# Performance work log

Hardware: AMD Instinct MI355X
Metric: run time of the kernel (lower is better)

## Reference

```python
import jax, jax.numpy as jnp
import numpy as np

N, E, NFEAT, NHID, NCLASS = 50000, 800000, 8, 128, 112
SMOOTH = 0.5          # smoo init arg
NEG_SLOPE_ATT = 0.2   # LeakyReLU slope inside sparse attention (SpGAT convention)
NEG_SLOPE_OUT = 0.01  # F.leaky_relu default in the outer loop
EPS = 1e-16


def setup_inputs() -> dict:
    key = jax.random.key(0)
    ks = jax.random.split(key, 12)
    g = lambda k, shape, s=0.1: jax.random.normal(k, shape, dtype=jnp.float32) * s
    return {
        "x": jax.random.normal(ks[0], (N, NFEAT), dtype=jnp.float32),
        "edge_index": jax.random.randint(ks[1], (2, E), 0, N, dtype=jnp.int64) if jax.config.jax_enable_x64 else jax.random.randint(ks[1], (2, E), 0, N, dtype=jnp.int32),
        "edge_weight": jax.random.uniform(ks[2], (E,), dtype=jnp.float32),
        # ScattterAttentionLayer 1: nfeat -> nhid (weight W, attention vector a split into src/dst halves)
        "W1": g(ks[3], (NFEAT, NHID)),
        "a1_src": g(ks[4], (NHID,)),
        "a1_dst": g(ks[5], (NHID,)),
        # ScattterAttentionLayer 2: nhid -> nhid
        "W2": g(ks[6], (NHID, NHID)),
        "a2_src": g(ks[7], (NHID,)),
        "a2_dst": g(ks[8], (NHID,)),
        # shared BatchNorm1d(nhid)
        "gamma": jnp.ones((NHID,), jnp.float32),
        "beta": jnp.zeros((NHID,), jnp.float32),
        # GC_withres: nhid -> nclass
        "Wg": g(ks[9], (NHID, NCLASS)),
        "bg": jnp.zeros((NCLASS,), jnp.float32),
    }


def scatter_attention(h_in, W, a_src, a_dst, src, dst):
    """Sparse GAT-style scatter attention (SpGraphAttentionLayer math).
    score_ij = exp(-leakyrelu(a_src.h_i + a_dst.h_j)); softmax-normalized per dst node."""
    h = h_in @ W                                   # [N, F]
    f_src = h @ a_src                              # [N]
    f_dst = h @ a_dst                              # [N]
    e = jnp.exp(-jax.nn.leaky_relu(f_src[src] + f_dst[dst], NEG_SLOPE_ATT))  # [E]
    denom = jax.ops.segment_sum(e, dst, num_segments=N) + EPS                # [N]
    num = jax.ops.segment_sum(e[:, None] * h[src], dst, num_segments=N)      # [N, F]
    return num / denom[:, None]


def batchnorm(x, gamma, beta):
    mu = x.mean(axis=0)
    var = x.var(axis=0)
    return (x - mu) * jax.lax.rsqrt(var + 1e-5) * gamma + beta


def reference(x, edge_index, edge_weight, W1, a1_src, a1_dst, W2, a2_src, a2_dst, gamma, beta, Wg, bg):
    src, dst = edge_index[0], edge_index[1]
    # conv loop (nlayers=3 -> two ScattterAttentionLayer convs), shared bn1, leaky_relu; dropout=identity (eval)
    h = scatter_attention(x, W1, a1_src, a1_dst, src, dst)
    h = jax.nn.leaky_relu(batchnorm(h, gamma, beta), NEG_SLOPE_OUT)
    h = scatter_attention(h, W2, a2_src, a2_dst, src, dst)
    h = jax.nn.leaky_relu(batchnorm(h, gamma, beta), NEG_SLOPE_OUT)
    # GC_withres: spmm((smooth*A + I)/(1+smooth), h @ Wg) + bias
    support = h @ Wg                               # [N, nclass]
    w = (SMOOTH / (1.0 + SMOOTH)) * edge_weight    # [E]
    agg = jax.ops.segment_sum(w[:, None] * support[src], dst, num_segments=N)
    return agg + support / (1.0 + SMOOTH) + bg
```

## Files before the change

### kernel.cpp

```cpp
#include <hip/hip_runtime.h>
#include <hip/hip_bf16.h>

#define N_NODES 50000
#define N_EDGES 800000
#define NFEAT   8
#define NHID    128
#define NCLASS  112
#define SEG_EPS 1e-16f
#define BN_EPS  1e-5f
#define CAP     64
#define MACRO_TILES 782
#define NODE_RANGE 6250
#define FILL_CHUNK 2048
#define FILL_CHUNKS 391
#define FSFD_BLOCKS 196
#define GATH_GRID 12800
#define ATT_GRID 3200
#define ATT_IT 4
#define Y1_BLOCKS 256

typedef __hip_bfloat16 bf16;
typedef __attribute__((ext_vector_type(8))) short short8;
typedef __attribute__((ext_vector_type(4))) float f32x4;
typedef __attribute__((ext_vector_type(4))) unsigned int u32x4;

__device__ __forceinline__ float bfbits2f(unsigned int lo16) {
    union { unsigned int u; float f; } c; c.u = lo16 << 16; return c.f;
}

__device__ __forceinline__ unsigned int pack_bf2(float a, float b) {
    union { unsigned int u; bf16 h[2]; } t;
    t.h[0] = __float2bfloat16(a);
    t.h[1] = __float2bfloat16(b);
    return t.u;
}

__global__ __launch_bounds__(256)
void k_fill_fsfd(const int* __restrict__ src, const int* __restrict__ dst,
                 const float* __restrict__ ewt,
                 int* __restrict__ cnt, unsigned int* __restrict__ bucket,
                 const float* __restrict__ x, const float* __restrict__ W1,
                 const float* __restrict__ a1s, const float* __restrict__ a1d,
                 float* __restrict__ fs, float* __restrict__ fd) {
    if (blockIdx.x < FILL_CHUNKS * 8) {
        const int range = blockIdx.x & 7;
        const int chunk = blockIdx.x >> 3;
        const int lo = range * NODE_RANGE, hi = lo + NODE_RANGE;
        const int e0 = chunk * FILL_CHUNK + threadIdx.x * 8;
        if (e0 >= N_EDGES) return;
        const int4 d0 = *(const int4*)&dst[e0];
        const int4 d1 = *(const int4*)&dst[e0 + 4];
        const int dd[8] = {d0.x, d0.y, d0.z, d0.w, d1.x, d1.y, d1.z, d1.w};
#pragma unroll
        for (int i = 0; i < 8; i++) {
            int d = dd[i];
            if (d < lo || d >= hi) continue;
            int e = e0 + i;
            int slot = atomicAdd(&cnt[d], 1);
            if (slot < CAP) {
                unsigned int iw = (unsigned int)(ewt[e] * 32767.f + 0.5f);
                bucket[d * CAP + slot] = ((unsigned int)src[e] << 15) | iw;
            }
        }
        return;
    }
    __shared__ float sw[16];
    const int t = threadIdx.x, w = t >> 6, lane = t & 63;
#pragma unroll
    for (int dd = 0; dd < 4; dd++) {
        int dot = w + dd * 4;
        int k = dot & 7;
        const float* a = (dot < 8) ? a1s : a1d;
        float v = W1[k * NHID + lane] * a[lane] + W1[k * NHID + 64 + lane] * a[64 + lane];
#pragma unroll
        for (int off = 32; off > 0; off >>= 1) v += __shfl_down(v, off);
        if (lane == 0) sw[dot] = v;
    }
    __syncthreads();
    const int i = (blockIdx.x - FILL_CHUNKS * 8) * 256 + t;
    if (i < N_NODES) {
        const float4 x0 = ((const float4*)x)[i * 2];
        const float4 x1 = ((const float4*)x)[i * 2 + 1];
        fs[i] = x0.x*sw[0] + x0.y*sw[1] + x0.z*sw[2] + x0.w*sw[3]
              + x1.x*sw[4] + x1.y*sw[5] + x1.z*sw[6] + x1.w*sw[7];
        fd[i] = x0.x*sw[8] + x0.y*sw[9] + x0.z*sw[10] + x0.w*sw[11]
              + x1.x*sw[12] + x1.y*sw[13] + x1.z*sw[14] + x1.w*sw[15];
    }
}

__global__ __launch_bounds__(256)
void k_sort_gather_x(const int* __restrict__ cnt, unsigned int* __restrict__ bucket,
                     const float* __restrict__ fs, const float* __restrict__ fd,
                     const float* __restrict__ x, float* __restrict__ xaggn) {
    const int xcd = blockIdx.x & 7;
    const int wb  = blockIdx.x >> 3;
    const int ni  = wb * 4 + (threadIdx.x >> 6);
    if (ni >= NODE_RANGE) return;
    const int d = xcd * NODE_RANGE + ni;
    const int lane = threadIdx.x & 63;
    const int deg = min(cnt[d], CAP);
    unsigned int v = (lane < deg) ? bucket[d * CAP + lane] : 0xFFFFFFFFu;
#pragma unroll
    for (int k = 2; k <= 64; k <<= 1) {
#pragma unroll
        for (int s = k >> 1; s > 0; s >>= 1) {
            unsigned int o = (unsigned int)__shfl_xor((int)v, s);
            bool keepmin = ((lane & s) == 0) == ((lane & k) == 0);
            v = keepmin ? min(v, o) : max(v, o);
        }
    }
    if (lane < deg) bucket[d * CAP + lane] = v;
    const int epair = lane >> 1;
    const int half  = lane & 1;
    const float fdd = fd[d];
    float4 acc = {0.f, 0.f, 0.f, 0.f};
    float den = 0.f;
    for (int base = 0; base < deg; base += 32) {
        int e = base + epair;
        unsigned int u = (unsigned int)__shfl((int)v, e);
        if (e < deg) {
            int s = u >> 15;
            float f = fs[s] + fdd;
            float lr = f > 0.f ? f : 0.2f * f;
            float c = __expf(-lr);
            if (half == 0) den += c;
            const float4 xv = *(const float4*)&x[s * NFEAT + half * 4];
            acc.x += c * xv.x; acc.y += c * xv.y; acc.z += c * xv.z; acc.w += c * xv.w;
        }
    }
#pragma unroll
    for (int off = 2; off < 64; off <<= 1) {
        acc.x += __shfl_xor(acc.x, off);
        acc.y += __shfl_xor(acc.y, off);
        acc.z += __shfl_xor(acc.z, off);
        acc.w += __shfl_xor(acc.w, off);
        den   += __shfl_xor(den, off);
    }
    den += __shfl_xor(den, 1);
    if (lane < 2) {
        float r = 1.f / (den + SEG_EPS);
        float4 o;
        o.x = acc.x * r; o.y = acc.y * r; o.z = acc.z * r; o.w = acc.w * r;
        *(float4*)&xaggn[d * NFEAT + half * 4] = o;
    }
}

__global__ __launch_bounds__(256)
void k_y1_gemm(const float* __restrict__ xaggn, const float* __restrict__ W1,
               bf16* __restrict__ y1, float* __restrict__ Psum, float* __restrict__ Psq) {
    int t = threadIdx.x;
    int r = t >> 7, j = t & 127;
    float w[NFEAT];
#pragma unroll
    for (int k = 0; k < NFEAT; k++) w[k] = W1[k * NHID + j];
    float ls = 0.f, lq = 0.f;
    for (int row = blockIdx.x * 2 + r; row < N_NODES; row += gridDim.x * 2) {
        const float4 x0 = ((const float4*)xaggn)[row * 2];
        const float4 x1 = ((const float4*)xaggn)[row * 2 + 1];
        float v = x0.x*w[0] + x0.y*w[1] + x0.z*w[2] + x0.w*w[3]
                + x1.x*w[4] + x1.y*w[5] + x1.z*w[6] + x1.w*w[7];
        y1[(size_t)row * NHID + j] = __float2bfloat16(v);
        ls += v; lq += v * v;
    }
    __shared__ float sbuf[256];
    sbuf[t] = ls; __syncthreads();
    if (r == 0) Psum[blockIdx.x * 128 + j] = sbuf[j] + sbuf[j + 128];
    __syncthreads();
    sbuf[t] = lq; __syncthreads();
    if (r == 0) Psq[blockIdx.x * 128 + j] = sbuf[j] + sbuf[j + 128];
}

__global__ __launch_bounds__(512)
void k_bn_w2(const float* __restrict__ Psum, const float* __restrict__ Psq,
             const float* __restrict__ gamma, const float* __restrict__ beta,
             float* __restrict__ scale, float* __restrict__ shift,
             const float* __restrict__ W2,
             const float* __restrict__ as_, const float* __restrict__ ad_,
             float* __restrict__ ws_, float* __restrict__ wd_) {
    const int t = threadIdx.x;
    if (blockIdx.x == 0) {
        int j = t & 127;
        int g = t >> 7;
        float s = 0.f, q = 0.f;
#pragma unroll 8
        for (int b = g * 64; b < g * 64 + 64; b++) {
            s += Psum[b * 128 + j];
            q += Psq[b * 128 + j];
        }
        __shared__ float Ls[4][128], Lq[4][128];
        Ls[g][j] = s; Lq[g][j] = q;
        __syncthreads();
        if (g == 0) {
            float st = ((Ls[0][j] + Ls[1][j]) + Ls[2][j]) + Ls[3][j];
            float qt = ((Lq[0][j] + Lq[1][j]) + Lq[2][j]) + Lq[3][j];
            float mu = st * (1.f / N_NODES);
            float var = qt * (1.f / N_NODES) - mu * mu;
            float rs = rsqrtf(var + BN_EPS);
            float ga = gamma[j];
            scale[j] = rs * ga;
            shift[j] = beta[j] - mu * rs * ga;
        }
        return;
    }
    const int k = (blockIdx.x - 1) * 4 + (t >> 7);
    const int n = t & 127;
    float wv = W2[k * NHID + n];
    float vs = wv * as_[n], vd = wv * ad_[n];
#pragma unroll
    for (int off = 32; off > 0; off >>= 1) { vs += __shfl_down(vs, off); vd += __shfl_down(vd, off); }
    __shared__ float ps[8], pd[8];
    const int wid = t >> 6;
    if ((t & 63) == 0) { ps[wid] = vs; pd[wid] = vd; }
    __syncthreads();
    if ((t & 127) == 0) { ws_[k] = ps[wid] + ps[wid + 1]; wd_[k] = pd[wid] + pd[wid + 1]; }
}

__global__ __launch_bounds__(256)
void k_reduce_a(const float* __restrict__ Psum, const float* __restrict__ Psq,
                int nIn, int chunk,
                float* __restrict__ Qsum, float* __restrict__ Qsq) {
    int j = threadIdx.x & 127;
    int h = threadIdx.x >> 7;
    int u = blockIdx.x * 2 + h;
    int b0 = u * chunk, b1 = min(b0 + chunk, nIn);
    float s = 0.f, q = 0.f;
#pragma unroll 8
    for (int b = b0; b < b1; b++) {
        s += Psum[b * 128 + j];
        q += Psq[b * 128 + j];
    }
    Qsum[u * 128 + j] = s;
    Qsq[u * 128 + j] = q;
}

__global__ __launch_bounds__(512)
void k_reduce_b(const float* __restrict__ Qsum, const float* __restrict__ Qsq,
                const float* __restrict__ gamma, const float* __restrict__ beta,
                float* __restrict__ scale, float* __restrict__ shift) {
    int j = threadIdx.x & 127;
    int g = threadIdx.x >> 7;
    float s = 0.f, q = 0.f;
#pragma unroll
    for (int u = g * 8; u < g * 8 + 8; u++) {
        s += Qsum[u * 128 + j];
        q += Qsq[u * 128 + j];
    }
    __shared__ float Ls[4][128], Lq[4][128];
    Ls[g][j] = s; Lq[g][j] = q;
    __syncthreads();
    if (g == 0) {
        float st = ((Ls[0][j] + Ls[1][j]) + Ls[2][j]) + Ls[3][j];
        float qt = ((Lq[0][j] + Lq[1][j]) + Lq[2][j]) + Lq[3][j];
        float mu = st * (1.f / N_NODES);
        float var = qt * (1.f / N_NODES) - mu * mu;
        float rs = rsqrtf(var + BN_EPS);
        float ga = gamma[j];
        scale[j] = rs * ga;
        shift[j] = beta[j] - mu * rs * ga;
    }
}

template<int NCV, int OSTRIDE, bool ATT>
__global__ __launch_bounds__(256)
void k_gemm_mfma(const bf16* __restrict__ Yin,
                 const float* __restrict__ scale, const float* __restrict__ shift,
                 const float* __restrict__ W,
                 bf16* __restrict__ hout,
                 const float* __restrict__ w2s, const float* __restrict__ w2d,
                 float* __restrict__ fs, float* __restrict__ fd) {
    constexpr int NT = NCV / 16;
    constexpr int NC4 = NCV / 4;
    __shared__ bf16 Wt[NCV * 136];
    __shared__ bf16 At[64 * 136];
    const int t = threadIdx.x;
    for (int idx = t; idx < 128 * NC4; idx += 256) {
        int k = idx / NC4, n4 = (idx - k * NC4) * 4;
        const float4 wv = *(const float4*)&W[k * NCV + n4];
        Wt[(n4 + 0) * 136 + k] = __float2bfloat16(wv.x);
        Wt[(n4 + 1) * 136 + k] = __float2bfloat16(wv.y);
        Wt[(n4 + 2) * 136 + k] = __float2bfloat16(wv.z);
        Wt[(n4 + 3) * 136 + k] = __float2bfloat16(wv.w);
    }
    const int chunk = t & 15;
    const int rgrp  = t >> 4;
    float sc[8], sh[8];
    {
        const float4 s0 = *(const float4*)&scale[chunk * 8];
        const float4 s1 = *(const float4*)&scale[chunk * 8 + 4];
        const float4 h0 = *(const float4*)&shift[chunk * 8];
        const float4 h1 = *(const float4*)&shift[chunk * 8 + 4];
        sc[0]=s0.x; sc[1]=s0.y; sc[2]=s0.z; sc[3]=s0.w;
        sc[4]=s1.x; sc[5]=s1.y; sc[6]=s1.z; sc[7]=s1.w;
        sh[0]=h0.x; sh[1]=h0.y; sh[2]=h0.z; sh[3]=h0.w;
        sh[4]=h1.x; sh[5]=h1.y; sh[6]=h1.z; sh[7]=h1.w;
    }
    const int lane = t & 63;
    const int m16 = lane & 15;
    const int g = lane >> 4;
    const int rg = t >> 6;
    short8 attb[4];
    if constexpr (ATT) {
#pragma unroll
        for (int kk = 0; kk < 4; kk++) {
            union { short8 s; unsigned int u[4]; } pk;
            if (m16 < 2) {
                const float* wv = (m16 == 0) ? w2s : w2d;
                const float4 f0 = *(const float4*)&wv[kk * 32 + g * 8];
                const float4 f1 = *(const float4*)&wv[kk * 32 + g * 8 + 4];
                pk.u[0] = pack_bf2(f0.x, f0.y);
                pk.u[1] = pack_bf2(f0.z, f0.w);
                pk.u[2] = pack_bf2(f1.x, f1.y);
                pk.u[3] = pack_bf2(f1.z, f1.w);
            } else {
                pk.u[0] = pk.u[1] = pk.u[2] = pk.u[3] = 0u;
            }
            attb[kk] = pk.s;
        }
    }
    __syncthreads();

    for (int mt = blockIdx.x; mt < MACRO_TILES; mt += gridDim.x) {
        const int row0 = mt * 64;
#pragma unroll
        for (int i2 = 0; i2 < 4; i2++) {
            int row = rgrp + i2 * 16;
            int grow = row0 + row;
            u32x4 u4 = (grow < N_NODES)
                ? *(const u32x4*)&((const unsigned int*)Yin)[(size_t)grow * 64 + chunk * 4]
                : (u32x4){0u, 0u, 0u, 0u};
            u32x4 pk;
#pragma unroll
            for (int fq = 0; fq < 4; fq++) {
                unsigned int u = u4[fq];
                float v0 = bfbits2f(u & 0xFFFF) * sc[2*fq]   + sh[2*fq];   v0 = v0 > 0.f ? v0 : 0.01f * v0;
                float v1 = bfbits2f(u >> 16)    * sc[2*fq+1] + sh[2*fq+1]; v1 = v1 > 0.f ? v1 : 0.01f * v1;
                pk[fq] = pack_bf2(v0, v1);
            }
            *(u32x4*)&At[row * 136 + chunk * 8] = pk;
        }
        __syncthreads();
        f32x4 acc[NT];
#pragma unroll
        for (int c = 0; c < NT; c++) acc[c] = (f32x4){0.f, 0.f, 0.f, 0.f};
        f32x4 accA = (f32x4){0.f, 0.f, 0.f, 0.f};
#pragma unroll
        for (int kk = 0; kk < 4; kk++) {
            short8 af = *(const short8*)&At[(rg * 16 + m16) * 136 + kk * 32 + g * 8];
#pragma unroll
            for (int c = 0; c < NT; c++) {
                short8 bfr = *(const short8*)&Wt[(c * 16 + m16) * 136 + kk * 32 + g * 8];
                acc[c] = __builtin_amdgcn_mfma_f32_16x16x32_bf16(af, bfr, acc[c], 0, 0, 0);
            }
            if constexpr (ATT)
                accA = __builtin_amdgcn_mfma_f32_16x16x32_bf16(af, attb[kk], accA, 0, 0, 0);
        }
        const int orow = row0 + rg * 16 + g * 4;
#pragma unroll
        for (int c = 0; c < NT; c++) {
#pragma unroll
            for (int r = 0; r < 4; r++) {
                int grow = orow + r;
                if (grow < N_NODES)
                    hout[(size_t)grow * OSTRIDE + c * 16 + m16] = __float2bfloat16(acc[c][r]);
            }
        }
        if constexpr (ATT) {
            if (m16 < 2) {
                float* o = (m16 == 0) ? fs : fd;
#pragma unroll
                for (int r = 0; r < 4; r++) {
                    int grow = orow + r;
                    if (grow < N_NODES) o[grow] = accA[r];
                }
            }
        }
        __syncthreads();
    }
}

__global__ __launch_bounds__(256)
void k_gather_attn_bf(const int* __restrict__ cnt, const unsigned int* __restrict__ bucket,
                      const float* __restrict__ fs, const float* __restrict__ fd,
                      const bf16* __restrict__ h, bf16* __restrict__ y,
                      float* __restrict__ Psum, float* __restrict__ Psq) {
    const int xcd = blockIdx.x & 7;
    const int wb  = blockIdx.x >> 3;
    const int t = threadIdx.x;
    const int q = t >> 6;
    const int lane = t & 63;
    const int grp = lane >> 4;
    const int l = lane & 15;
    __shared__ int s_idx[4][CAP];
    __shared__ float s_e[4][CAP];
    __shared__ float sred[4][16][8];
    float ls[8], lq[8];
#pragma unroll
    for (int i = 0; i < 8; i++) { ls[i] = 0.f; lq[i] = 0.f; }

    for (int it = 0; it < ATT_IT; it++) {
        const int ni = (wb + it * 400) * 4 + q;
        if (ni >= NODE_RANGE) continue;
        const int d = xcd * NODE_RANGE + ni;
        const int deg = min(cnt[d], CAP);
        const float fdd = fd[d];
        if (lane < deg) {
            int s = bucket[d * CAP + lane] >> 15;
            float f = fs[s] + fdd;
            float lr = f > 0.f ? f : 0.2f * f;
            s_idx[q][lane] = s;
            s_e[q][lane] = __expf(-lr);
        }
        float a[8];
#pragma unroll
        for (int i = 0; i < 8; i++) a[i] = 0.f;
        float den = 0.f;
#pragma unroll 2
        for (int base = 0; base < deg; base += 4) {
            int k = base + grp;
            bool ev = k < deg;
            int kk = ev ? k : 0;
            float e = ev ? s_e[q][kk] : 0.f;
            int sidx = s_idx[q][kk];
            u32x4 u4 = *(const u32x4*)&((const unsigned int*)h)[(size_t)sidx * 64 + l * 4];
            den += e;
#pragma unroll
            for (int fq = 0; fq < 4; fq++) {
                unsigned int u = u4[fq];
                a[2*fq]   += e * bfbits2f(u & 0xFFFF);
                a[2*fq+1] += e * bfbits2f(u >> 16);
            }
        }
#pragma unroll
        for (int off = 16; off < 64; off <<= 1) {
#pragma unroll
            for (int i = 0; i < 8; i++) a[i] += __shfl_xor(a[i], off);
            den += __shfl_xor(den, off);
        }
        float r = 1.f / (den + SEG_EPS);
        if (lane < 16) {
            u32x4 pk;
#pragma unroll
            for (int fq = 0; fq < 4; fq++) {
                float v0 = a[2*fq] * r, v1 = a[2*fq+1] * r;
                pk[fq] = pack_bf2(v0, v1);
                ls[2*fq] += v0;   lq[2*fq] += v0 * v0;
                ls[2*fq+1] += v1; lq[2*fq+1] += v1 * v1;
            }
            *(u32x4*)&((unsigned int*)y)[(size_t)d * 64 + l * 4] = pk;
        }
    }
    if (lane < 16) {
#pragma unroll
        for (int i = 0; i < 8; i++) sred[q][l][i] = ls[i];
    }
    __syncthreads();
    if (t < 128) {
        int l16 = t >> 3, i8 = t & 7;
        Psum[blockIdx.x * 128 + t] =
            ((sred[0][l16][i8] + sred[1][l16][i8]) + sred[2][l16][i8]) + sred[3][l16][i8];
    }
    __syncthreads();
    if (lane < 16) {
#pragma unroll
        for (int i = 0; i < 8; i++) sred[q][l][i] = lq[i];
    }
    __syncthreads();
    if (t < 128) {
        int l16 = t >> 3, i8 = t & 7;
        Psq[blockIdx.x * 128 + t] =
            ((sred[0][l16][i8] + sred[1][l16][i8]) + sred[2][l16][i8]) + sred[3][l16][i8];
    }
}

__global__ __launch_bounds__(256)
void k_gather_out_bf(const int* __restrict__ cnt, const unsigned int* __restrict__ bucket,
                     const bf16* __restrict__ sup, const float* __restrict__ bg,
                     float* __restrict__ out) {
    const int xcd = blockIdx.x & 7;
    const int wb  = blockIdx.x >> 3;
    const int ni  = wb * 4 + (threadIdx.x >> 6);
    if (ni >= NODE_RANGE) return;
    const int d = xcd * NODE_RANGE + ni;
    const int t = threadIdx.x;
    const int q = t >> 6;
    const int lane = t & 63;
    const int grp = lane >> 4;
    const int l = lane & 15;
    __shared__ int s_idx[4][CAP];
    __shared__ float s_w[4][CAP];
    const int deg = min(cnt[d], CAP);
    if (lane < deg) {
        unsigned int b = bucket[d * CAP + lane];
        s_idx[q][lane] = b >> 15;
        s_w[q][lane] = (float)(b & 0x7FFF) * (1.f / (32767.f * 3.f));
    }
    float a[8];
#pragma unroll
    for (int i = 0; i < 8; i++) a[i] = 0.f;
#pragma unroll 2
    for (int base = 0; base < deg; base += 4) {
        int k = base + grp;
        bool ev = k < deg;
        int kk = ev ? k : 0;
        float w = ev ? s_w[q][kk] : 0.f;
        int sidx = s_idx[q][kk];
        u32x4 u4 = *(const u32x4*)&((const unsigned int*)sup)[(size_t)sidx * 64 + l * 4];
#pragma unroll
        for (int fq = 0; fq < 4; fq++) {
            unsigned int u = u4[fq];
            a[2*fq]   += w * bfbits2f(u & 0xFFFF);
            a[2*fq+1] += w * bfbits2f(u >> 16);
        }
    }
#pragma unroll
    for (int off = 16; off < 64; off <<= 1) {
#pragma unroll
        for (int i = 0; i < 8; i++) a[i] += __shfl_xor(a[i], off);
    }
    if (l < 14) {
        u32x4 us = *(const u32x4*)&((const unsigned int*)sup)[(size_t)d * 64 + l * 4];
        const float4 b0 = *(const float4*)&bg[l * 8];
        const float4 b1 = *(const float4*)&bg[l * 8 + 4];
        float4 o0, o1;
        o0.x = a[0] + bfbits2f(us[0] & 0xFFFF) * (2.f/3.f) + b0.x;
        o0.y = a[1] + bfbits2f(us[0] >> 16)    * (2.f/3.f) + b0.y;
        o0.z = a[2] + bfbits2f(us[1] & 0xFFFF) * (2.f/3.f) + b0.z;
        o0.w = a[3] + bfbits2f(us[1] >> 16)    * (2.f/3.f) + b0.w;
        o1.x = a[4] + bfbits2f(us[2] & 0xFFFF) * (2.f/3.f) + b1.x;
        o1.y = a[5] + bfbits2f(us[2] >> 16)    * (2.f/3.f) + b1.y;
        o1.z = a[6] + bfbits2f(us[3] & 0xFFFF) * (2.f/3.f) + b1.z;
        o1.w = a[7] + bfbits2f(us[3] >> 16)    * (2.f/3.f) + b1.w;
        *(float4*)&out[(size_t)d * NCLASS + l * 8]     = o0;
        *(float4*)&out[(size_t)d * NCLASS + l * 8 + 4] = o1;
    }
}

extern "C" void kernel_launch(void* const* d_in, const int* in_sizes, int n_in,
                              void* d_out, int out_size, void* d_ws, size_t ws_size,
                              hipStream_t stream) {
    const float* x    = (const float*)d_in[0];
    const int*   ei   = (const int*)d_in[1];
    const float* ewt  = (const float*)d_in[2];
    const float* W1   = (const float*)d_in[3];
    const float* a1s  = (const float*)d_in[4];
    const float* a1d  = (const float*)d_in[5];
    const float* W2   = (const float*)d_in[6];
    const float* a2s  = (const float*)d_in[7];
    const float* a2d  = (const float*)d_in[8];
    const float* gam  = (const float*)d_in[9];
    const float* bet  = (const float*)d_in[10];
    const float* Wg   = (const float*)d_in[11];
    const float* bg   = (const float*)d_in[12];
    float* out = (float*)d_out;

    const int* src = ei;
    const int* dst = ei + N_EDGES;

    float* ws    = (float*)d_ws;
    bf16*  Yb    = (bf16*)ws;
    bf16*  Hb    = (bf16*)(ws + 3203072);
    unsigned int* bucket = (unsigned int*)(ws + 6403072);
    float* xagg  = ws + 9603072;
    float* fs    = ws + 10003072;
    float* fd    = ws + 10053072;
    int*   cnt   = (int*)(ws + 10103072);
    float* scale = ws + 10153072;
    float* shift = scale + 128;
    float* w2s   = shift + 128;
    float* w2d   = w2s + 128;
    float* Psum  = ws + 10153600;
    float* Psq   = Psum + 409600;
    float* Qsum  = Psq + 409600;
    float* Qsq   = Qsum + 4096;

    hipMemsetAsync(cnt, 0, (size_t)N_NODES * 4, stream);
    k_fill_fsfd<<<FILL_CHUNKS * 8 + FSFD_BLOCKS, 256, 0, stream>>>(
        src, dst, ewt, cnt, bucket, x, W1, a1s, a1d, fs, fd);

    k_sort_gather_x<<<GATH_GRID, 256, 0, stream>>>(cnt, bucket, fs, fd, x, xagg);
    k_y1_gemm<<<Y1_BLOCKS, 256, 0, stream>>>(xagg, W1, Yb, Psum, Psq);
    k_bn_w2<<<33, 512, 0, stream>>>(Psum, Psq, gam, bet, scale, shift,
                                    W2, a2s, a2d, w2s, w2d);

    k_gemm_mfma<128, 128, true><<<MACRO_TILES, 256, 0, stream>>>(Yb, scale, shift, W2, Hb,
                                                                 w2s, w2d, fs, fd);
    k_gather_attn_bf<<<ATT_GRID, 256, 0, stream>>>(cnt, bucket, fs, fd, Hb, Yb,
                                                   Psum, Psq);
    k_reduce_a<<<16, 256, 0, stream>>>(Psum, Psq, ATT_GRID, 100, Qsum, Qsq);
    k_reduce_b<<<1, 512, 0, stream>>>(Qsum, Qsq, gam, bet, scale, shift);

    k_gemm_mfma<112, 128, false><<<MACRO_TILES, 256, 0, stream>>>(Yb, scale, shift, Wg, Hb,
                                                                  nullptr, nullptr, nullptr, nullptr);
    k_gather_out_bf<<<GATH_GRID, 256, 0, stream>>>(cnt, bucket, Hb, bg, out);
}
```

Baseline: 319.8 us.

## Pre-transpose weights to bf16 once and load GEMM A operands directly from global

Weight transpose and bf16 conversion for W2 and Wg move into the small BN kernel via extra blocks, so each of the 782 GEMM blocks only does vector copies of a pre-transposed weight instead of scattered per-element conversion stores. The GEMM drops the LDS staging of the activation tile and its barriers: each lane loads its MFMA A fragment straight from global memory and applies BN and leaky-ReLU in registers, with scale and shift kept in shared memory. The two gather kernels also raise their inner-loop unroll from 2 to 4. Trade-offs: A-fragment global loads are less coalesced than the old staged tile loads, and the workspace needs space for the extra transposed weights.

```diff
diff --git a/kernel.cpp b/kernel.cpp
--- a/kernel.cpp
+++ b/kernel.cpp
@@ -176,7 +176,9 @@
              float* __restrict__ scale, float* __restrict__ shift,
              const float* __restrict__ W2,
              const float* __restrict__ as_, const float* __restrict__ ad_,
-             float* __restrict__ ws_, float* __restrict__ wd_) {
+             float* __restrict__ ws_, float* __restrict__ wd_,
+             const float* __restrict__ Wg,
+             bf16* __restrict__ W2t, bf16* __restrict__ Wgt) {
     const int t = threadIdx.x;
     if (blockIdx.x == 0) {
         int j = t & 127;
@@ -202,17 +204,33 @@
         }
         return;
     }
-    const int k = (blockIdx.x - 1) * 4 + (t >> 7);
-    const int n = t & 127;
-    float wv = W2[k * NHID + n];
-    float vs = wv * as_[n], vd = wv * ad_[n];
-#pragma unroll
-    for (int off = 32; off > 0; off >>= 1) { vs += __shfl_down(vs, off); vd += __shfl_down(vd, off); }
-    __shared__ float ps[8], pd[8];
-    const int wid = t >> 6;
-    if ((t & 63) == 0) { ps[wid] = vs; pd[wid] = vd; }
-    __syncthreads();
-    if ((t & 127) == 0) { ws_[k] = ps[wid] + ps[wid + 1]; wd_[k] = pd[wid] + pd[wid + 1]; }
+    if (blockIdx.x < 33) {
+        const int k = (blockIdx.x - 1) * 4 + (t >> 7);
+        const int n = t & 127;
+        float wv = W2[k * NHID + n];
+        float vs = wv * as_[n], vd = wv * ad_[n];
+#pragma unroll
+        for (int off = 32; off > 0; off >>= 1) { vs += __shfl_down(vs, off); vd += __shfl_down(vd, off); }
+        __shared__ float ps[8], pd[8];
+        const int wid = t >> 6;
+        if ((t & 63) == 0) { ps[wid] = vs; pd[wid] = vd; }
+        __syncthreads();
+        if ((t & 127) == 0) { ws_[k] = ps[wid] + ps[wid + 1]; wd_[k] = pd[wid] + pd[wid + 1]; }
+        return;
+    }
+    if (blockIdx.x < 49) {
+        const int n = (blockIdx.x - 33) * 8 + (t >> 6);
+        const int k2 = (t & 63) * 2;
+        float v0 = W2[k2 * NHID + n];
+        float v1 = W2[(k2 + 1) * NHID + n];
+        *(unsigned int*)&W2t[n * 128 + k2] = pack_bf2(v0, v1);
+        return;
+    }
+    const int n = (blockIdx.x - 49) * 8 + (t >> 6);
+    const int k2 = (t & 63) * 2;
+    float v0 = Wg[k2 * NCLASS + n];
+    float v1 = Wg[(k2 + 1) * NCLASS + n];
+    *(unsigned int*)&Wgt[n * 128 + k2] = pack_bf2(v0, v1);
 }
 
 __global__ __launch_bounds__(256)
@@ -260,40 +278,23 @@
     }
 }
 
-template<int NCV, int OSTRIDE, bool ATT>
+template<int NCV, bool ATT>
 __global__ __launch_bounds__(256)
 void k_gemm_mfma(const bf16* __restrict__ Yin,
                  const float* __restrict__ scale, const float* __restrict__ shift,
-                 const float* __restrict__ W,
+                 const bf16* __restrict__ Wt_g,
                  bf16* __restrict__ hout,
                  const float* __restrict__ w2s, const float* __restrict__ w2d,
                  float* __restrict__ fs, float* __restrict__ fd) {
     constexpr int NT = NCV / 16;
-    constexpr int NC4 = NCV / 4;
     __shared__ bf16 Wt[NCV * 136];
-    __shared__ bf16 At[64 * 136];
+    __shared__ float scb[128], shb[128];
     const int t = threadIdx.x;
-    for (int idx = t; idx < 128 * NC4; idx += 256) {
-        int k = idx / NC4, n4 = (idx - k * NC4) * 4;
-        const float4 wv = *(const float4*)&W[k * NCV + n4];
-        Wt[(n4 + 0) * 136 + k] = __float2bfloat16(wv.x);
-        Wt[(n4 + 1) * 136 + k] = __float2bfloat16(wv.y);
-        Wt[(n4 + 2) * 136 + k] = __float2bfloat16(wv.z);
-        Wt[(n4 + 3) * 136 + k] = __float2bfloat16(wv.w);
-    }
-    const int chunk = t & 15;
-    const int rgrp  = t >> 4;
-    float sc[8], sh[8];
-    {
-        const float4 s0 = *(const float4*)&scale[chunk * 8];
-        const float4 s1 = *(const float4*)&scale[chunk * 8 + 4];
-        const float4 h0 = *(const float4*)&shift[chunk * 8];
-        const float4 h1 = *(const float4*)&shift[chunk * 8 + 4];
-        sc[0]=s0.x; sc[1]=s0.y; sc[2]=s0.z; sc[3]=s0.w;
-        sc[4]=s1.x; sc[5]=s1.y; sc[6]=s1.z; sc[7]=s1.w;
-        sh[0]=h0.x; sh[1]=h0.y; sh[2]=h0.z; sh[3]=h0.w;
-        sh[4]=h1.x; sh[5]=h1.y; sh[6]=h1.z; sh[7]=h1.w;
-    }
+    for (int idx = t; idx < NCV * 16; idx += 256) {
+        int n = idx >> 4, c = idx & 15;
+        *(u32x4*)&Wt[n * 136 + c * 8] = *(const u32x4*)&Wt_g[n * 128 + c * 8];
+    }
+    if (t < 128) { scb[t] = scale[t]; shb[t] = shift[t]; }
     const int lane = t & 63;
     const int m16 = lane & 15;
     const int g = lane >> 4;
@@ -319,62 +320,59 @@
     }
     __syncthreads();
 
-    for (int mt = blockIdx.x; mt < MACRO_TILES; mt += gridDim.x) {
-        const int row0 = mt * 64;
-#pragma unroll
-        for (int i2 = 0; i2 < 4; i2++) {
-            int row = rgrp + i2 * 16;
-            int grow = row0 + row;
-            u32x4 u4 = (grow < N_NODES)
-                ? *(const u32x4*)&((const unsigned int*)Yin)[(size_t)grow * 64 + chunk * 4]
-                : (u32x4){0u, 0u, 0u, 0u};
-            u32x4 pk;
-#pragma unroll
-            for (int fq = 0; fq < 4; fq++) {
-                unsigned int u = u4[fq];
-                float v0 = bfbits2f(u & 0xFFFF) * sc[2*fq]   + sh[2*fq];   v0 = v0 > 0.f ? v0 : 0.01f * v0;
-                float v1 = bfbits2f(u >> 16)    * sc[2*fq+1] + sh[2*fq+1]; v1 = v1 > 0.f ? v1 : 0.01f * v1;
-                pk[fq] = pack_bf2(v0, v1);
-            }
-            *(u32x4*)&At[row * 136 + chunk * 8] = pk;
-        }
-        __syncthreads();
-        f32x4 acc[NT];
-#pragma unroll
-        for (int c = 0; c < NT; c++) acc[c] = (f32x4){0.f, 0.f, 0.f, 0.f};
-        f32x4 accA = (f32x4){0.f, 0.f, 0.f, 0.f};
-#pragma unroll
-        for (int kk = 0; kk < 4; kk++) {
-            short8 af = *(const short8*)&At[(rg * 16 + m16) * 136 + kk * 32 + g * 8];
-#pragma unroll
-            for (int c = 0; c < NT; c++) {
-                short8 bfr = *(const short8*)&Wt[(c * 16 + m16) * 136 + kk * 32 + g * 8];
-                acc[c] = __builtin_amdgcn_mfma_f32_16x16x32_bf16(af, bfr, acc[c], 0, 0, 0);
-            }
-            if constexpr (ATT)
-                accA = __builtin_amdgcn_mfma_f32_16x16x32_bf16(af, attb[kk], accA, 0, 0, 0);
-        }
-        const int orow = row0 + rg * 16 + g * 4;
+    const int row0 = blockIdx.x * 64;
+    const int arow = row0 + rg * 16 + m16;
+    const bool rok = arow < N_NODES;
+    f32x4 acc[NT];
+#pragma unroll
+    for (int c = 0; c < NT; c++) acc[c] = (f32x4){0.f, 0.f, 0.f, 0.f};
+    f32x4 accA = (f32x4){0.f, 0.f, 0.f, 0.f};
+#pragma unroll
+    for (int kk = 0; kk < 4; kk++) {
+        u32x4 u4 = rok
+            ? *(const u32x4*)&((const unsigned int*)Yin)[(size_t)arow * 64 + kk * 16 + g * 4]
+            : (u32x4){0u, 0u, 0u, 0u};
+        const float4 s0 = *(const float4*)&scb[kk * 32 + g * 8];
+        const float4 s1 = *(const float4*)&scb[kk * 32 + g * 8 + 4];
+        const float4 h0 = *(const float4*)&shb[kk * 32 + g * 8];
+        const float4 h1 = *(const float4*)&shb[kk * 32 + g * 8 + 4];
+        const float scv[8] = {s0.x, s0.y, s0.z, s0.w, s1.x, s1.y, s1.z, s1.w};
+        const float shv[8] = {h0.x, h0.y, h0.z, h0.w, h1.x, h1.y, h1.z, h1.w};
+        union { short8 s; unsigned int u[4]; } A;
+#pragma unroll
+        for (int fq = 0; fq < 4; fq++) {
+            unsigned int u = u4[fq];
+            float v0 = bfbits2f(u & 0xFFFF) * scv[2*fq]   + shv[2*fq];   v0 = v0 > 0.f ? v0 : 0.01f * v0;
+            float v1 = bfbits2f(u >> 16)    * scv[2*fq+1] + shv[2*fq+1]; v1 = v1 > 0.f ? v1 : 0.01f * v1;
+            A.u[fq] = pack_bf2(v0, v1);
+        }
 #pragma unroll
         for (int c = 0; c < NT; c++) {
+            short8 bfr = *(const short8*)&Wt[(c * 16 + m16) * 136 + kk * 32 + g * 8];
+            acc[c] = __builtin_amdgcn_mfma_f32_16x16x32_bf16(A.s, bfr, acc[c], 0, 0, 0);
+        }
+        if constexpr (ATT)
+            accA = __builtin_amdgcn_mfma_f32_16x16x32_bf16(A.s, attb[kk], accA, 0, 0, 0);
+    }
+    const int orow = row0 + rg * 16 + g * 4;
+#pragma unroll
+    for (int c = 0; c < NT; c++) {
+#pragma unroll
+        for (int r = 0; r < 4; r++) {
+            int grow = orow + r;
+            if (grow < N_NODES)
+                hout[(size_t)grow * 128 + c * 16 + m16] = __float2bfloat16(acc[c][r]);
+        }
+    }
+    if constexpr (ATT) {
+        if (m16 < 2) {
+            float* o = (m16 == 0) ? fs : fd;
 #pragma unroll
             for (int r = 0; r < 4; r++) {
                 int grow = orow + r;
-                if (grow < N_NODES)
-                    hout[(size_t)grow * OSTRIDE + c * 16 + m16] = __float2bfloat16(acc[c][r]);
+                if (grow < N_NODES) o[grow] = accA[r];
             }
         }
-        if constexpr (ATT) {
-            if (m16 < 2) {
-                float* o = (m16 == 0) ? fs : fd;
-#pragma unroll
-                for (int r = 0; r < 4; r++) {
-                    int grow = orow + r;
-                    if (grow < N_NODES) o[grow] = accA[r];
-                }
-            }
-        }
-        __syncthreads();
     }
 }
 
@@ -414,7 +412,7 @@
 #pragma unroll
         for (int i = 0; i < 8; i++) a[i] = 0.f;
         float den = 0.f;
-#pragma unroll 2
+#pragma unroll 4
         for (int base = 0; base < deg; base += 4) {
             int k = base + grp;
             bool ev = k < deg;
@@ -497,7 +495,7 @@
     float a[8];
 #pragma unroll
     for (int i = 0; i < 8; i++) a[i] = 0.f;
-#pragma unroll 2
+#pragma unroll 4
     for (int base = 0; base < deg; base += 4) {
         int k = base + grp;
         bool ev = k < deg;
@@ -572,6 +570,8 @@
     float* Psq   = Psum + 409600;
     float* Qsum  = Psq + 409600;
     float* Qsq   = Qsum + 4096;
+    bf16*  W2t   = (bf16*)(ws + 10980992);
+    bf16*  Wgt   = W2t + 16384;
 
     hipMemsetAsync(cnt, 0, (size_t)N_NODES * 4, stream);
     k_fill_fsfd<<<FILL_CHUNKS * 8 + FSFD_BLOCKS, 256, 0, stream>>>(
@@ -579,17 +579,17 @@
 
     k_sort_gather_x<<<GATH_GRID, 256, 0, stream>>>(cnt, bucket, fs, fd, x, xagg);
     k_y1_gemm<<<Y1_BLOCKS, 256, 0, stream>>>(xagg, W1, Yb, Psum, Psq);
-    k_bn_w2<<<33, 512, 0, stream>>>(Psum, Psq, gam, bet, scale, shift,
-                                    W2, a2s, a2d, w2s, w2d);
-
-    k_gemm_mfma<128, 128, true><<<MACRO_TILES, 256, 0, stream>>>(Yb, scale, shift, W2, Hb,
-                                                                 w2s, w2d, fs, fd);
+    k_bn_w2<<<63, 512, 0, stream>>>(Psum, Psq, gam, bet, scale, shift,
+                                    W2, a2s, a2d, w2s, w2d, Wg, W2t, Wgt);
+
+    k_gemm_mfma<128, true><<<MACRO_TILES, 256, 0, stream>>>(Yb, scale, shift, W2t, Hb,
+                                                            w2s, w2d, fs, fd);
     k_gather_attn_bf<<<ATT_GRID, 256, 0, stream>>>(cnt, bucket, fs, fd, Hb, Yb,
                                                    Psum, Psq);
     k_reduce_a<<<16, 256, 0, stream>>>(Psum, Psq, ATT_GRID, 100, Qsum, Qsq);
     k_reduce_b<<<1, 512, 0, stream>>>(Qsum, Qsq, gam, bet, scale, shift);
 
-    k_gemm_mfma<112, 128, false><<<MACRO_TILES, 256, 0, stream>>>(Yb, scale, shift, Wg, Hb,
-                                                                  nullptr, nullptr, nullptr, nullptr);
+    k_gemm_mfma<112, false><<<MACRO_TILES, 256, 0, stream>>>(Yb, scale, shift, Wgt, Hb,
+                                                             nullptr, nullptr, nullptr, nullptr);
     k_gather_out_bf<<<GATH_GRID, 256, 0, stream>>>(cnt, bucket, Hb, bg, out);
 }
```

Result: faster. 299.2 us (-6.4%).
